# Kernel tuning notes

Hardware: AMD Instinct MI355X
Metric: run time of the kernel (lower is better)

## Reference

```python
import jax, jax.numpy as jnp
import numpy as np

NUM_HEADS = 8


def setup_inputs() -> dict:
    key = jax.random.key(0)
    ks = jax.random.split(key, 9)
    B, S, E = 16, 2048, 768
    s = 0.02
    return {
        "features": jax.random.normal(ks[0], (B, S, E), jnp.float32),
        "in_proj_w": jax.random.normal(ks[1], (3 * E, E), jnp.float32) * s,
        "in_proj_b": jnp.zeros((3 * E,), jnp.float32),
        "out_proj_w": jax.random.normal(ks[2], (E, E), jnp.float32) * s,
        "out_proj_b": jnp.zeros((E,), jnp.float32),
        "w1": jax.random.normal(ks[3], (384, E), jnp.float32) * s,
        "b1": jnp.zeros((384,), jnp.float32),
        "w2": jax.random.normal(ks[4], (1, 384), jnp.float32) * s,
        "b2": jnp.zeros((1,), jnp.float32),
    }


def reference(features, in_proj_w, in_proj_b, out_proj_w, out_proj_b, w1, b1, w2, b2):
    # torch nn.MultiheadAttention default batch_first=False: dim 0 is the
    # attended sequence axis (length B here), dim 1 is the MHA batch (S).
    B, S, E = features.shape
    H = NUM_HEADS
    Dh = E // H
    qkv = features @ in_proj_w.T + in_proj_b          # (B, S, 3E)
    q, k, v = jnp.split(qkv, 3, axis=-1)
    q = q.reshape(B, S, H, Dh)
    k = k.reshape(B, S, H, Dh)
    v = v.reshape(B, S, H, Dh)
    scale = 1.0 / jnp.sqrt(jnp.asarray(Dh, features.dtype))
    # attention over axis-0 positions (l, m in 0..B-1), per (s, h)
    scores = jnp.einsum('lshd,mshd->shlm', q * scale, k)
    attn = jax.nn.softmax(scores, axis=-1)
    ctx = jnp.einsum('shlm,mshd->lshd', attn, v).reshape(B, S, E)
    attn_out = ctx @ out_proj_w.T + out_proj_b        # (B, S, E)
    # batched 2-layer MLP (replaces the Python per-row loop)
    h = jax.nn.relu(attn_out @ w1.T + b1)             # (B, S, 384)
    prob = h @ w2.T + b2                              # (B, S, 1)
    contacts = jnp.broadcast_to(prob, (B, S, S))      # contacts[:, i, :] = prob[:, i]
    return contacts
```

## Files before the change

### kernel.cpp

```cpp
#include <hip/hip_runtime.h>

typedef unsigned short u16;
typedef __attribute__((ext_vector_type(8))) __bf16 bf16x8;
typedef __attribute__((ext_vector_type(4))) float floatx4;

#define B_DIM  16
#define S_DIM  2048
#define E_DIM  768
#define HEADS  8
#define DHEAD  96
#define MROWS  32768
#define QKV_LD 2304
#define ATT_ST 392
#define NT     12

#define GLDS(gp, lp) __builtin_amdgcn_global_load_lds( \
    (const __attribute__((address_space(1))) void*)(gp), \
    (__attribute__((address_space(3))) void*)(lp), 16, 0, 0)

__device__ __forceinline__ u16 f2b(float f) {
    unsigned u = __float_as_uint(f);
    u += 0x7fffu + ((u >> 16) & 1u);
    return (u16)(u >> 16);
}
__device__ __forceinline__ float blo(unsigned u) { return __uint_as_float(u << 16); }
__device__ __forceinline__ float bhi(unsigned u) { return __uint_as_float(u & 0xffff0000u); }

__device__ __forceinline__ void axpy8(float* acc, float p, uint4 v) {
    acc[0] += p * blo(v.x); acc[1] += p * bhi(v.x);
    acc[2] += p * blo(v.y); acc[3] += p * bhi(v.y);
    acc[4] += p * blo(v.z); acc[5] += p * bhi(v.z);
    acc[6] += p * blo(v.w); acc[7] += p * bhi(v.w);
}

__device__ __forceinline__ bf16x8 ldsw(const u16* half_base, int rowh, int cb) {
    return *(const bf16x8*)((const char*)half_base + rowh * 128 + (cb ^ ((rowh & 7) << 4)));
}

#define PB0 24576
#define PB1 26304
#define PB2 26592
#define PB3 27168
#define PB4 27552
__global__ __launch_bounds__(256) void prep(const float* __restrict__ features,
                                            const float* __restrict__ in_proj_w,
                                            const float* __restrict__ w1,
                                            const float* __restrict__ out_proj_w,
                                            const float* __restrict__ bo,
                                            const float* __restrict__ b1,
                                            u16* __restrict__ fbf, u16* __restrict__ wib,
                                            u16* __restrict__ w1b, u16* __restrict__ WoT,
                                            float* __restrict__ cbuf) {
    __shared__ float tsh[32][33];
    const int b = blockIdx.x, tid = threadIdx.x;
    if (b < PB2) {
        const float* src; u16* dst; long i;
        if (b < PB0)      { src = features;  dst = fbf; i = (long)b * 256 + tid; }
        else if (b < PB1) { src = in_proj_w; dst = wib; i = (long)(b - PB0) * 256 + tid; }
        else              { src = w1;        dst = w1b; i = (long)(b - PB1) * 256 + tid; }
        float4 f = ((const float4*)src)[i];
        ushort4 r;
        r.x = f2b(f.x); r.y = f2b(f.y); r.z = f2b(f.z); r.w = f2b(f.w);
        ((ushort4*)dst)[i] = r;
    } else if (b < PB3) {
        const int t = b - PB2;
        const int bxT = t % 24, byT = t / 24;
        const int tx = tid & 31, ty = tid >> 5;
        int x = bxT * 32 + tx;
        int y = byT * 32 + ty;
#pragma unroll
        for (int j = 0; j < 4; j++) tsh[ty + j * 8][tx] = out_proj_w[(long)(y + j * 8) * 768 + x];
        __syncthreads();
        x = byT * 32 + tx;
        y = bxT * 32 + ty;
#pragma unroll
        for (int j = 0; j < 4; j++) WoT[(long)(y + j * 8) * 768 + x] = f2b(tsh[tx][ty + j * 8]);
    } else {
        const int n = b - PB3;
        const float* row = w1 + (long)n * 768;
        float s = row[tid] * bo[tid] + row[tid + 256] * bo[tid + 256] + row[tid + 512] * bo[tid + 512];
#pragma unroll
        for (int off = 32; off > 0; off >>= 1) s += __shfl_xor(s, off);
        if ((tid & 63) == 0) tsh[0][tid >> 6] = s;
        __syncthreads();
        if (tid == 0) cbuf[n] = tsh[0][0] + tsh[0][1] + tsh[0][2] + tsh[0][3] + b1[n];
    }
}

__global__ __launch_bounds__(512, 2) void qkv256(const u16* __restrict__ A,
                                                 const u16* __restrict__ W,
                                                 const float* __restrict__ bias,
                                                 u16* __restrict__ Cout,
                                                 const u16* __restrict__ gA,
                                                 const u16* __restrict__ gW,
                                                 u16* __restrict__ gC) {
    __shared__ __align__(16) u16 lds[2 * 32768];
    const int tid = threadIdx.x;
    const int bx  = blockIdx.x;
    int bm, bn, ldc, Mvalid; const u16 *Aa, *Ww; const float* bs; u16* Co; bool perm;
    if (bx < 1152) {
        const int xcd = bx & 7;
        const int q   = bx >> 3;
        bn = q % 9;
        bm = (q / 9) * 8 + xcd;
        Aa = A; Ww = W; bs = bias; Co = Cout; ldc = QKV_LD; perm = true; Mvalid = 1 << 30;
    } else {
        const int g = bx - 1152;
        bn = g % 3; bm = g / 3;
        Aa = gA; Ww = gW; bs = nullptr; Co = gC; ldc = 768; perm = false; Mvalid = 384;
    }
    const int r0 = tid >> 3,        r1 = (tid + 512) >> 3;
    const int q0 = (tid & 7) ^ (r0 & 7), q1 = ((tid + 512) & 7) ^ (r1 & 7);
    const u16* pA0 = Aa + (long)(bm * 256 + r0) * 768 + q0 * 8;
    const u16* pA1 = Aa + (long)(bm * 256 + r1) * 768 + q1 * 8;
    const u16* pB0 = Ww + (long)(bn * 256 + r0) * 768 + q0 * 8;
    const u16* pB1 = Ww + (long)(bn * 256 + r1) * 768 + q1 * 8;
    u16* dA0 = lds + tid * 8;
    u16* dA1 = lds + 4096 + tid * 8;
    u16* dB0 = lds + 16384 + tid * 8;
    u16* dB1 = lds + 16384 + 4096 + tid * 8;

#define IS_A(h, p, t) do { \
    GLDS(pA0 + (h) * 98304 + (t) * 64, dA0 + (p) * 32768 + (h) * 8192); \
    GLDS(pA1 + (h) * 98304 + (t) * 64, dA1 + (p) * 32768 + (h) * 8192); } while (0)
#define IS_B(h, p, t) do { \
    GLDS(pB0 + (h) * 98304 + (t) * 64, dB0 + (p) * 32768 + (h) * 8192); \
    GLDS(pB1 + (h) * 98304 + (t) * 64, dB1 + (p) * 32768 + (h) * 8192); } while (0)
#define MFMA_PRE() do { \
    __builtin_amdgcn_s_barrier(); \
    asm volatile("s_waitcnt lgkmcnt(0)" ::: "memory"); \
    __builtin_amdgcn_sched_barrier(0); \
    __builtin_amdgcn_s_setprio(1); } while (0)
#define MFMA_POST() do { \
    __builtin_amdgcn_s_setprio(0); \
    __builtin_amdgcn_s_barrier(); } while (0)

    const int lane = tid & 63, wid = tid >> 6;
    const int wr = wid >> 2, wc = wid & 3;
    const int fr = lane & 15, fg = lane >> 4;
    const int fq2 = fg * 16;
    const int wb  = (wc & 1) * 64;
    const u16* bufA_base = lds + wr * 8192;
    const u16* bufB_base = lds + 16384 + (wc >> 1) * 8192;

    IS_A(0, 0, 0); IS_A(1, 0, 0); IS_B(0, 0, 0); IS_B(1, 0, 0);
    IS_A(0, 1, 1); IS_A(1, 1, 1);
    asm volatile("s_waitcnt vmcnt(4)" ::: "memory");
    __builtin_amdgcn_s_barrier();

    floatx4 acc[8][4] = {};
#pragma unroll 2
    for (int t = 0; t < NT; ++t) {
        const int p = t & 1, pn = p ^ 1;
        const u16* bA = bufA_base + p * 32768;
        const u16* bB = bufB_base + p * 32768;
        bf16x8 aF[4], bF[4];
#pragma unroll
        for (int i = 0; i < 4; ++i) aF[i] = ldsw(bA, i * 16 + fr, fq2);
#pragma unroll
        for (int j = 0; j < 4; ++j) bF[j] = ldsw(bB, wb + j * 16 + fr, fq2);
        if (t + 1 < NT) IS_B(0, pn, t + 1);
        MFMA_PRE();
#pragma unroll
        for (int i = 0; i < 4; ++i)
#pragma unroll
            for (int j = 0; j < 4; ++j)
                acc[i][j] = __builtin_amdgcn_mfma_f32_16x16x32_bf16(aF[i], bF[j], acc[i][j], 0, 0, 0);
        MFMA_POST();
#pragma unroll
        for (int i = 0; i < 4; ++i) aF[i] = ldsw(bA, (i + 4) * 16 + fr, fq2);
        if (t + 1 < NT) IS_B(1, pn, t + 1);
        MFMA_PRE();
#pragma unroll
        for (int i = 0; i < 4; ++i)
#pragma unroll
            for (int j = 0; j < 4; ++j)
                acc[i + 4][j] = __builtin_amdgcn_mfma_f32_16x16x32_bf16(aF[i], bF[j], acc[i + 4][j], 0, 0, 0);
        MFMA_POST();
#pragma unroll
        for (int i = 0; i < 4; ++i) aF[i] = ldsw(bA, i * 16 + fr, 64 + fq2);
#pragma unroll
        for (int j = 0; j < 4; ++j) bF[j] = ldsw(bB, wb + j * 16 + fr, 64 + fq2);
        MFMA_PRE();
#pragma unroll
        for (int i = 0; i < 4; ++i)
#pragma unroll
            for (int j = 0; j < 4; ++j)
                acc[i][j] = __builtin_amdgcn_mfma_f32_16x16x32_bf16(aF[i], bF[j], acc[i][j], 0, 0, 0);
        MFMA_POST();
#pragma unroll
        for (int i = 0; i < 4; ++i) aF[i] = ldsw(bA, (i + 4) * 16 + fr, 64 + fq2);
        MFMA_PRE();
#pragma unroll
        for (int i = 0; i < 4; ++i)
#pragma unroll
            for (int j = 0; j < 4; ++j)
                acc[i + 4][j] = __builtin_amdgcn_mfma_f32_16x16x32_bf16(aF[i], bF[j], acc[i + 4][j], 0, 0, 0);
        MFMA_POST();
        if (t + 2 < NT) {
            IS_A(0, p, t + 2); IS_A(1, p, t + 2);
            asm volatile("s_waitcnt vmcnt(4)" ::: "memory");
            __builtin_amdgcn_s_barrier();
        } else if (t + 1 < NT) {
            asm volatile("s_waitcnt vmcnt(0)" ::: "memory");
            __builtin_amdgcn_s_barrier();
        }
    }

    const int rq = fg * 4;
    float bvj[4];
#pragma unroll
    for (int j = 0; j < 4; ++j) bvj[j] = bs ? bs[bn * 256 + wc * 64 + j * 16 + fr] : 0.f;
    u16* strip = lds + wid * 2048;
    const int sr = lane >> 3, sc = lane & 7;
#pragma unroll
    for (int pass = 0; pass < 4; ++pass) {
#pragma unroll
        for (int ii = 0; ii < 2; ++ii) {
            const int i = pass * 2 + ii;
#pragma unroll
            for (int j = 0; j < 4; ++j)
#pragma unroll
                for (int r = 0; r < 4; ++r)
                    strip[(ii * 16 + rq + r) * 64 + j * 16 + fr] = f2b(acc[i][j][r] + bvj[j]);
        }
#pragma unroll
        for (int it = 0; it < 4; ++it) {
            const int lr = it * 8 + sr;
            uint4 v = *(const uint4*)(strip + lr * 64 + sc * 8);
            const int rl = bm * 256 + wr * 128 + pass * 32 + lr;
            if (rl < Mvalid) {
                const long grow = perm ? (long)(((rl & 2047) << 4) | (rl >> 11)) : (long)rl;
                *(uint4*)(Co + grow * ldc + bn * 256 + wc * 64 + sc * 8) = v;
            }
        }
    }
#undef IS_A
#undef IS_B
#undef MFMA_PRE
#undef MFMA_POST
}

__global__ __launch_bounds__(256) void attn_kernel(u16* __restrict__ qkv) {
    __shared__ __align__(16) u16 sQ[16 * ATT_ST], sK[16 * ATT_ST], sV[16 * ATT_ST];
    __shared__ float sS[4][16][16];
    const int tid = threadIdx.x;
    const int bx  = blockIdx.x;
    const int xcd   = bx & 7;
    const int hh    = (bx >> 3) & 1;
    const int inner = bx >> 4;
    const int s = (xcd << 8) | inner;
    const u16* base = qkv + (long)s * 16 * QKV_LD + hh * 384;

#pragma unroll
    for (int it = 0; it < 9; it++) {
        const int i = it * 256 + tid;
        const int t = i / 768, rem = i % 768, l = rem / 48, c = rem % 48;
        const u16* src = base + (long)l * QKV_LD + t * E_DIM + c * 8;
        u16* dst = (t == 0 ? sQ : t == 1 ? sK : sV) + l * ATT_ST + c * 8;
        *(uint4*)dst = *(const uint4*)src;
    }
    __syncthreads();

    const int lane = tid & 63;
    const int w    = tid >> 6;
    const int fr   = lane & 15;
    const int fq   = (lane >> 4) * 8;
    floatx4 acc = {};
    const u16* qrow = sQ + fr * ATT_ST + w * DHEAD + fq;
    const u16* krow = sK + fr * ATT_ST + w * DHEAD + fq;
#pragma unroll
    for (int st = 0; st < 3; st++) {
        bf16x8 qa = *(const bf16x8*)(qrow + st * 32);
        bf16x8 kb = *(const bf16x8*)(krow + st * 32);
        acc = __builtin_amdgcn_mfma_f32_16x16x32_bf16(qa, kb, acc, 0, 0, 0);
    }
    const int rq = (lane >> 4) * 4;
#pragma unroll
    for (int r = 0; r < 4; r++) {
        float sc = acc[r] * 0.10206207261596577f;
        float mx = sc;
#pragma unroll
        for (int off = 8; off > 0; off >>= 1) mx = fmaxf(mx, __shfl_xor(mx, off));
        float e = __expf(sc - mx);
        float sum = e;
#pragma unroll
        for (int off = 8; off > 0; off >>= 1) sum += __shfl_xor(sum, off);
        sS[w][rq + r][fr] = e / sum;
    }
    __syncthreads();

#pragma unroll
    for (int j = 0; j < 3; j++) {
        const int task = j * 256 + tid;
        const int h = task / 192, rem = task % 192, ll = rem / 12, c = rem % 12;
        float a[8] = {};
#pragma unroll
        for (int mm = 0; mm < 16; mm++) {
            const float p = sS[h][ll][mm];
            uint4 vw = *(const uint4*)(sV + mm * ATT_ST + h * DHEAD + c * 8);
            axpy8(a, p, vw);
        }
        ushort4 o0, o1;
        o0.x = f2b(a[0]); o0.y = f2b(a[1]); o0.z = f2b(a[2]); o0.w = f2b(a[3]);
        o1.x = f2b(a[4]); o1.y = f2b(a[5]); o1.z = f2b(a[6]); o1.w = f2b(a[7]);
        u16* dst = qkv + ((long)s * 16 + ll) * QKV_LD + (hh * 4 + h) * DHEAD + c * 8;
        *(ushort4*)dst = o0;
        *(ushort4*)(dst + 4) = o1;
    }
}

__global__ __launch_bounds__(256) void mlp_gemm(const u16* __restrict__ A, int lda,
                                                const u16* __restrict__ G,
                                                const float* __restrict__ cbias,
                                                const float* __restrict__ w2,
                                                float* __restrict__ part) {
    __shared__ __align__(16) u16 sA[2 * 128 * 32];
    __shared__ __align__(16) u16 sB[2 * 128 * 32];
    __shared__ float rowsum[128];
    const int tid = threadIdx.x;
    const int bx  = blockIdx.x;
    const int xcd = bx & 7;
    const int q   = bx >> 3;
    const int bn  = q % 3;
    const int t   = q / 3;
    const int bm  = (xcd << 5) | t;
    if (tid < 128) rowsum[tid] = 0.f;
    const int lane = tid & 63;
    const int wid  = tid >> 6;
    const int wm   = (wid >> 1) * 64;
    const int wn   = (wid & 1) * 64;
    const int ar = tid >> 2;
    const int ac = (tid & 3) * 8;
    const u16* Ap = A + (long)(bm * 128 + ar) * lda + ac;
    const u16* Wp = G + (long)(bn * 128 + ar) * 768 + ac;
    const long a2 = (long)64 * lda;
    const long w2s = (long)64 * 768;
    const int fr = lane & 15;
    const int fq = (lane >> 4) * 8;
    const int rq = (lane >> 4) * 4;

    floatx4 acc[4][4] = {};
    for (int k0 = 0; k0 < 768; k0 += 64) {
#pragma unroll
        for (int h = 0; h < 2; h++) {
            GLDS(Ap + k0 + h * 32,       sA + h * 4096 + tid * 8);
            GLDS(Ap + a2 + k0 + h * 32,  sA + h * 4096 + 2048 + tid * 8);
            GLDS(Wp + k0 + h * 32,       sB + h * 4096 + tid * 8);
            GLDS(Wp + w2s + k0 + h * 32, sB + h * 4096 + 2048 + tid * 8);
        }
        __syncthreads();
#pragma unroll
        for (int h = 0; h < 2; h++) {
            bf16x8 aF[4], bF[4];
#pragma unroll
            for (int i = 0; i < 4; i++) {
                aF[i] = *(const bf16x8*)(sA + h * 4096 + (wm + i * 16 + fr) * 32 + fq);
                bF[i] = *(const bf16x8*)(sB + h * 4096 + (wn + i * 16 + fr) * 32 + fq);
            }
#pragma unroll
            for (int i = 0; i < 4; i++)
#pragma unroll
                for (int j = 0; j < 4; j++)
                    acc[i][j] = __builtin_amdgcn_mfma_f32_16x16x32_bf16(aF[i], bF[j], acc[i][j], 0, 0, 0);
        }
        __syncthreads();
    }
    float partl[4][4] = {};
#pragma unroll
    for (int j = 0; j < 4; j++) {
        const int col = bn * 128 + wn + j * 16 + fr;
        const float cv = cbias[col];
        const float wv = w2[col];
#pragma unroll
        for (int i = 0; i < 4; i++)
#pragma unroll
            for (int r = 0; r < 4; r++)
                partl[i][r] += fmaxf(acc[i][j][r] + cv, 0.f) * wv;
    }
#pragma unroll
    for (int i = 0; i < 4; i++)
#pragma unroll
        for (int r = 0; r < 4; r++) {
            float v = partl[i][r];
#pragma unroll
            for (int off = 8; off > 0; off >>= 1) v += __shfl_xor(v, off);
            if (fr == 0) atomicAdd(&rowsum[wm + i * 16 + rq + r], v);
        }
    __syncthreads();
    if (tid < 128) part[(long)bn * MROWS + bm * 128 + tid] = rowsum[tid];
}

__global__ __launch_bounds__(256) void bcast_kernel(const float* __restrict__ part,
                                                    const float* __restrict__ b2,
                                                    float* __restrict__ out) {
    const int tid = threadIdx.x;
    const long s  = blockIdx.x;
    const float b2v = b2[0];
#pragma unroll
    for (int l = 0; l < 16; l++) {
        const long p = s * 16 + l;
        const float pv = part[p] + part[MROWS + p] + part[2 * MROWS + p] + b2v;
        floatx4 v4 = {pv, pv, pv, pv};
        floatx4* dst = (floatx4*)(out + ((long)l * S_DIM + s) * S_DIM);
        __builtin_nontemporal_store(v4, dst + tid);
        __builtin_nontemporal_store(v4, dst + tid + 256);
    }
}

extern "C" void kernel_launch(void* const* d_in, const int* in_sizes, int n_in,
                              void* d_out, int out_size, void* d_ws, size_t ws_size,
                              hipStream_t stream) {
    const float* features   = (const float*)d_in[0];
    const float* in_proj_b  = (const float*)d_in[2];
    const float* out_proj_b = (const float*)d_in[4];
    const float* b1 = (const float*)d_in[6];
    const float* w2 = (const float*)d_in[7];
    const float* b2 = (const float*)d_in[8];
    float* out = (float*)d_out;

    char* p = (char*)d_ws;
    u16* fbf = (u16*)p; p += (size_t)MROWS * E_DIM * 2;
    u16* wib = (u16*)p; p += (size_t)QKV_LD * E_DIM * 2;
    u16* w1b = (u16*)p; p += (size_t)384 * E_DIM * 2;
    u16* WoT = (u16*)p; p += (size_t)E_DIM * E_DIM * 2;
    u16* Gbf = (u16*)p; p += (size_t)384 * E_DIM * 2;
    float* cbuf  = (float*)p; p += 384 * 4;
    float* partb = (float*)p; p += (size_t)3 * MROWS * 4;
    p = (char*)(((size_t)p + 255) & ~(size_t)255);
    u16* qkv = (u16*)p; p += (size_t)MROWS * QKV_LD * 2;
    u16* ctx = qkv;

    prep<<<PB4, 256, 0, stream>>>(features, (const float*)d_in[1], (const float*)d_in[5],
                                  (const float*)d_in[3], out_proj_b, b1,
                                  fbf, wib, w1b, WoT, cbuf);
    qkv256<<<1158, 512, 0, stream>>>(fbf, wib, in_proj_b, qkv, w1b, WoT, Gbf);
    attn_kernel<<<S_DIM * 2, 256, 0, stream>>>(qkv);
    mlp_gemm<<<768, 256, 0, stream>>>(ctx, QKV_LD, Gbf, cbuf, w2, partb);
    bcast_kernel<<<S_DIM, 256, 0, stream>>>(partb, b2, out);
}
```

Baseline: 555.0 us.

## Swizzle attention LDS layout with direct global-to-LDS loads and pad GEMM epilogue strip

The attention kernel now loads Q/K/V straight into LDS with global_load_lds, no longer staging through registers. It uses an XOR-swizzled 384-element row layout in place of the padded 392 stride, so MFMA operand reads and V reads avoid bank conflicts. The output store is packed into one 16-byte write instead of two 8-byte writes. The GEMM epilogue strip gets a 72-element padded stride to reduce LDS bank conflicts, which needs more LDS per wave and risks overflowing the allocated buffer if it was sized exactly.

```diff
diff --git a/kernel.cpp b/kernel.cpp
--- a/kernel.cpp
+++ b/kernel.cpp
@@ -11,7 +11,6 @@
 #define DHEAD  96
 #define MROWS  32768
 #define QKV_LD 2304
-#define ATT_ST 392
 #define NT     12
 
 #define GLDS(gp, lp) __builtin_amdgcn_global_load_lds( \
@@ -211,7 +210,7 @@
     float bvj[4];
 #pragma unroll
     for (int j = 0; j < 4; ++j) bvj[j] = bs ? bs[bn * 256 + wc * 64 + j * 16 + fr] : 0.f;
-    u16* strip = lds + wid * 2048;
+    u16* strip = lds + wid * 2304;
     const int sr = lane >> 3, sc = lane & 7;
 #pragma unroll
     for (int pass = 0; pass < 4; ++pass) {
@@ -222,12 +221,12 @@
             for (int j = 0; j < 4; ++j)
 #pragma unroll
                 for (int r = 0; r < 4; ++r)
-                    strip[(ii * 16 + rq + r) * 64 + j * 16 + fr] = f2b(acc[i][j][r] + bvj[j]);
+                    strip[(ii * 16 + rq + r) * 72 + j * 16 + fr] = f2b(acc[i][j][r] + bvj[j]);
         }
 #pragma unroll
         for (int it = 0; it < 4; ++it) {
             const int lr = it * 8 + sr;
-            uint4 v = *(const uint4*)(strip + lr * 64 + sc * 8);
+            uint4 v = *(const uint4*)(strip + lr * 72 + sc * 8);
             const int rl = bm * 256 + wr * 128 + pass * 32 + lr;
             if (rl < Mvalid) {
                 const long grow = perm ? (long)(((rl & 2047) << 4) | (rl >> 11)) : (long)rl;
@@ -242,7 +241,7 @@
 }
 
 __global__ __launch_bounds__(256) void attn_kernel(u16* __restrict__ qkv) {
-    __shared__ __align__(16) u16 sQ[16 * ATT_ST], sK[16 * ATT_ST], sV[16 * ATT_ST];
+    __shared__ __align__(16) u16 sQKV[3 * 16 * 384];
     __shared__ float sS[4][16][16];
     const int tid = threadIdx.x;
     const int bx  = blockIdx.x;
@@ -254,28 +253,28 @@
 
 #pragma unroll
     for (int it = 0; it < 9; it++) {
-        const int i = it * 256 + tid;
-        const int t = i / 768, rem = i % 768, l = rem / 48, c = rem % 48;
-        const u16* src = base + (long)l * QKV_LD + t * E_DIM + c * 8;
-        u16* dst = (t == 0 ? sQ : t == 1 ? sK : sV) + l * ATT_ST + c * 8;
-        *(uint4*)dst = *(const uint4*)src;
+        const int id = it * 256 + tid;
+        const int t = id / 768, within = id % 768;
+        const int l = within / 48, c = within % 48;
+        const int csrc = c ^ (l & 7);
+        GLDS(base + (long)l * QKV_LD + t * E_DIM + csrc * 8, sQKV + id * 8);
     }
     __syncthreads();
 
     const int lane = tid & 63;
     const int w    = tid >> 6;
     const int fr   = lane & 15;
-    const int fq   = (lane >> 4) * 8;
+    const int fg   = lane >> 4;
     floatx4 acc = {};
-    const u16* qrow = sQ + fr * ATT_ST + w * DHEAD + fq;
-    const u16* krow = sK + fr * ATT_ST + w * DHEAD + fq;
 #pragma unroll
     for (int st = 0; st < 3; st++) {
-        bf16x8 qa = *(const bf16x8*)(qrow + st * 32);
-        bf16x8 kb = *(const bf16x8*)(krow + st * 32);
+        const int ch  = w * 12 + st * 4 + fg;
+        const int chs = ch ^ (fr & 7);
+        bf16x8 qa = *(const bf16x8*)(sQKV + fr * 384 + chs * 8);
+        bf16x8 kb = *(const bf16x8*)(sQKV + 6144 + fr * 384 + chs * 8);
         acc = __builtin_amdgcn_mfma_f32_16x16x32_bf16(qa, kb, acc, 0, 0, 0);
     }
-    const int rq = (lane >> 4) * 4;
+    const int rq = fg * 4;
 #pragma unroll
     for (int r = 0; r < 4; r++) {
         float sc = acc[r] * 0.10206207261596577f;
@@ -298,15 +297,16 @@
 #pragma unroll
         for (int mm = 0; mm < 16; mm++) {
             const float p = sS[h][ll][mm];
-            uint4 vw = *(const uint4*)(sV + mm * ATT_ST + h * DHEAD + c * 8);
+            const int ch = (h * 12 + c) ^ (mm & 7);
+            uint4 vw = *(const uint4*)(sQKV + 12288 + mm * 384 + ch * 8);
             axpy8(a, p, vw);
         }
-        ushort4 o0, o1;
-        o0.x = f2b(a[0]); o0.y = f2b(a[1]); o0.z = f2b(a[2]); o0.w = f2b(a[3]);
-        o1.x = f2b(a[4]); o1.y = f2b(a[5]); o1.z = f2b(a[6]); o1.w = f2b(a[7]);
-        u16* dst = qkv + ((long)s * 16 + ll) * QKV_LD + (hh * 4 + h) * DHEAD + c * 8;
-        *(ushort4*)dst = o0;
-        *(ushort4*)(dst + 4) = o1;
+        uint4 o;
+        o.x = (unsigned)f2b(a[0]) | ((unsigned)f2b(a[1]) << 16);
+        o.y = (unsigned)f2b(a[2]) | ((unsigned)f2b(a[3]) << 16);
+        o.z = (unsigned)f2b(a[4]) | ((unsigned)f2b(a[5]) << 16);
+        o.w = (unsigned)f2b(a[6]) | ((unsigned)f2b(a[7]) << 16);
+        *(uint4*)(qkv + ((long)s * 16 + ll) * QKV_LD + (hh * 4 + h) * DHEAD + c * 8) = o;
     }
 }
 
```

Result: no change. 552.1 us (-0.5%).
